# Kernel tuning notes

Measured on AMD Instinct MI355X. Metric: run time of the kernel, lower is better.

## Reference

```python
import jax, jax.numpy as jnp
from jax import lax
import numpy as np

B, N_MEL, T_MEL = 256, 80, 800
R = 16                      # n_frames_per_step
RNN = 1024                  # decoder_rnn_dim
ENC = 256                   # token_embedding_size
MEL_DIM = N_MEL * R         # 1280, == RNN + ENC (LSTMCell input size)
IN_DIM = RNN + ENC          # 1280


def setup_inputs() -> dict:
    key = jax.random.key(0)
    ks = jax.random.split(key, 10)
    s = 0.02
    return {
        "context": jax.random.normal(ks[0], (B, ENC), dtype=jnp.float32),
        "target": jax.random.normal(ks[1], (B, N_MEL, T_MEL), dtype=jnp.float32),
        "W_ih": jax.random.normal(ks[2], (4 * RNN, IN_DIM), dtype=jnp.float32) * s,
        "b_ih": jnp.zeros((4 * RNN,), dtype=jnp.float32),
        "W_hh": jax.random.normal(ks[3], (4 * RNN, RNN), dtype=jnp.float32) * s,
        "b_hh": jnp.zeros((4 * RNN,), dtype=jnp.float32),
        "W_proj": jax.random.normal(ks[4], (MEL_DIM, IN_DIM), dtype=jnp.float32) * s,
        "b_proj": jnp.zeros((MEL_DIM,), dtype=jnp.float32),
        "W_gate": jax.random.normal(ks[5], (1, IN_DIM), dtype=jnp.float32) * s,
        "b_gate": jnp.zeros((1,), dtype=jnp.float32),
    }


def _decoder_forward(context, target, W_ih, b_ih, W_hh, b_hh, W_proj, b_proj, W_gate, b_gate):
    b = context.shape[0]
    n_mel, t_mel = target.shape[1], target.shape[2]
    mel_dim = W_proj.shape[0]
    r = mel_dim // n_mel                      # n_frames_per_step
    T = t_mel // r                            # decoder steps
    rnn = W_hh.shape[1]

    # parse_decoder_inputs: [B, n_mel, T_mel] -> [T, B, mel_dim]
    frames = target.transpose(0, 2, 1).reshape(b, T, mel_dim).transpose(1, 0, 2)
    # step 0 uses the all-zeros go frame; step t>=1 uses target frame t (teacher forcing, p=1)
    inputs = frames.at[0].set(0.0)

    h0 = jnp.zeros((b, rnn), dtype=context.dtype)
    c0 = jnp.zeros((b, rnn), dtype=context.dtype)

    def step(carry, x):
        h, c = carry
        gates = x @ W_ih.T + b_ih + h @ W_hh.T + b_hh   # [B, 4*rnn]
        i, f, g, o = jnp.split(gates, 4, axis=-1)        # torch LSTMCell gate order
        c_new = jax.nn.sigmoid(f) * c + jax.nn.sigmoid(i) * jnp.tanh(g)
        h_new = jax.nn.sigmoid(o) * jnp.tanh(c_new)
        # eval mode: dropout on c is identity
        oc = jnp.concatenate([h_new, context], axis=1)   # [B, rnn+enc]
        mel = oc @ W_proj.T + b_proj                     # [B, mel_dim]
        gate = oc @ W_gate.T + b_gate                    # [B, 1]
        return (h_new, c_new), (mel, gate)

    _, (mels, gates) = lax.scan(step, (h0, c0), inputs)
    # mels: [T, B, mel_dim] -> [B, n_mel, T_mel]
    mel_outputs = mels.transpose(1, 0, 2).reshape(b, T * r, n_mel).transpose(0, 2, 1)
    gate_outputs = gates.transpose(1, 0, 2)              # [B, T, 1]
    return mel_outputs, gate_outputs


def reference(context, target, W_ih, b_ih, W_hh, b_hh, W_proj, b_proj, W_gate, b_gate):
    return _decoder_forward(context, target, W_ih, b_ih, W_hh, b_hh,
                            W_proj, b_proj, W_gate, b_gate)
```

## Files before the change

kernel.cpp:

```cpp
#include <hip/hip_runtime.h>
#include <hip/hip_bf16.h>
#include <math.h>

#define BB     256
#define NMEL   80
#define TMEL   800
#define NFR    16
#define TT     50
#define RNN    1024
#define ENC    256
#define INDIM  1280
#define G4     4096
#define MROWS  (TT*BB)

typedef __attribute__((ext_vector_type(8))) short bf16x8;
typedef __attribute__((ext_vector_type(4))) float f32x4;

#define GAS __attribute__((address_space(1)))
#define LAS __attribute__((address_space(3)))

__device__ __forceinline__ unsigned short f2bf(float f) {
    unsigned int u = __float_as_uint(f);
    u += 0x7FFFu + ((u >> 16) & 1u);
    return (unsigned short)(u >> 16);
}
__device__ __forceinline__ float bf2f(unsigned short s) {
    return __uint_as_float(((unsigned int)s) << 16);
}
__device__ __forceinline__ float fsig(float x) {
    return 1.f / (1.f + __expf(-x));
}
__device__ __forceinline__ float ftanh(float x) {
    return 2.f / (1.f + __expf(-2.f * x)) - 1.f;
}


__global__ void k_f32_to_bf16(const float* __restrict__ src,
                              unsigned short* __restrict__ dst, int n) {
    for (int i = blockIdx.x * blockDim.x + threadIdx.x; i < n;
         i += gridDim.x * blockDim.x)
        dst[i] = f2bf(src[i]);
}

__global__ void k_conv_wph(const float* __restrict__ wproj,
                           unsigned short* __restrict__ dst) {
    const int n = INDIM * RNN;
    for (int i = blockIdx.x * blockDim.x + threadIdx.x; i < n;
         i += gridDim.x * blockDim.x) {
        int mp = i >> 10, k = i & 1023;
        int mel = mp >> 4, fr = mp & 15;
        dst[i] = f2bf(wproj[(fr * NMEL + mel) * INDIM + k]);
    }
}

__global__ void k_frames(const float* __restrict__ target,
                         unsigned short* __restrict__ frames) {
    const int n = TT * BB * INDIM;
    for (int i = blockIdx.x * blockDim.x + threadIdx.x; i < n;
         i += gridDim.x * blockDim.x) {
        int k = i % INDIM;
        int rb = i / INDIM;
        int b = rb & (BB - 1);
        int t = rb >> 8;
        unsigned short v = 0;
        if (t > 0) {
            int mel = k % NMEL, fr = k / NMEL;
            v = f2bf(target[(b * NMEL + mel) * TMEL + t * NFR + fr]);
        }
        frames[i] = v;
    }
}

__global__ void k_ctxproj(const float* __restrict__ context,
                          const float* __restrict__ wproj,
                          const float* __restrict__ bproj,
                          float* __restrict__ ctx) {
    int i = blockIdx.x * blockDim.x + threadIdx.x;
    if (i >= BB * INDIM) return;
    int mp = i % INDIM, b = i / INDIM;
    int mel = mp >> 4, fr = mp & 15;
    int m = fr * NMEL + mel;
    const float* wr = wproj + (size_t)m * INDIM + RNN;
    const float* cb = context + b * ENC;
    float acc = bproj[m];
    for (int e = 0; e < ENC; ++e) acc += cb[e] * wr[e];
    ctx[(size_t)b * INDIM + mp] = acc;
}

__global__ void k_gatectx(const float* __restrict__ context,
                          const float* __restrict__ wgate,
                          const float* __restrict__ bgate,
                          float* __restrict__ gctx) {
    int b = blockIdx.x * blockDim.x + threadIdx.x;
    if (b >= BB) return;
    float acc = bgate[0];
    const float* cb = context + b * ENC;
    for (int e = 0; e < ENC; ++e) acc += cb[e] * wgate[RNN + e];
    gctx[b] = acc;
}

template<int STRIDE, int KDIM>
__device__ __forceinline__ void gemm_core2(const unsigned short* __restrict__ A,
                                           const unsigned short* __restrict__ Bw,
                                           int mblk, int nblk,
                                           unsigned short* As,
                                           unsigned short* Bs,
                                           f32x4 acc[4][2]) {
    const int tid = threadIdx.x, lane = tid & 63, w = tid >> 6;
    const int lr = lane & 15, q = lane >> 4;
    const int wm = (w >> 2) * 64, wn = (w & 3) * 32;
    const int cc1 = tid, cc2 = tid + 512;
    const int r1 = cc1 >> 3, s1 = ((cc1 & 7) ^ (r1 & 7)) * 8;
    const int r2 = cc2 >> 3, s2 = ((cc2 & 7) ^ (r2 & 7)) * 8;
    const unsigned short* a1p = A + (size_t)(mblk + r1) * STRIDE + s1;
    const unsigned short* a2p = A + (size_t)(mblk + r2) * STRIDE + s2;
    const unsigned short* b1p = Bw + (size_t)(nblk + r1) * STRIDE + s1;
    const unsigned short* b2p = Bw + (size_t)(nblk + r2) * STRIDE + s2;

#define GSTAGE(buf, k0) do {                                                   \
    __builtin_amdgcn_global_load_lds((const GAS unsigned int*)(a1p + (k0)),    \
        (LAS unsigned int*)(As + (buf) * 8192 + w * 512), 16, 0, 0);           \
    __builtin_amdgcn_global_load_lds((const GAS unsigned int*)(a2p + (k0)),    \
        (LAS unsigned int*)(As + (buf) * 8192 + 4096 + w * 512), 16, 0, 0);    \
    __builtin_amdgcn_global_load_lds((const GAS unsigned int*)(b1p + (k0)),    \
        (LAS unsigned int*)(Bs + (buf) * 8192 + w * 512), 16, 0, 0);           \
    __builtin_amdgcn_global_load_lds((const GAS unsigned int*)(b2p + (k0)),    \
        (LAS unsigned int*)(Bs + (buf) * 8192 + 4096 + w * 512), 16, 0, 0); } while (0)

    constexpr int NIT = KDIM / 64;
    GSTAGE(0, 0);
    #pragma unroll 4
    for (int it = 0; it < NIT; ++it) {
        if (it < NIT - 1) {
            GSTAGE((it + 1) & 1, (it + 1) * 64);
            asm volatile("s_waitcnt vmcnt(4)" ::: "memory");
        } else {
            asm volatile("s_waitcnt vmcnt(0)" ::: "memory");
        }
        asm volatile("s_barrier" ::: "memory");
        __builtin_amdgcn_sched_barrier(0);
        const unsigned short* Ab = As + (it & 1) * 8192;
        const unsigned short* Bb = Bs + (it & 1) * 8192;
        #pragma unroll
        for (int ks = 0; ks < 2; ++ks) {
            const int j = (((ks * 4 + q) ^ (lr & 7)) * 8);
            bf16x8 af[4], bv[2];
            #pragma unroll
            for (int mi = 0; mi < 4; ++mi)
                af[mi] = *(const bf16x8*)(Ab + (wm + mi * 16 + lr) * 64 + j);
            #pragma unroll
            for (int ni = 0; ni < 2; ++ni)
                bv[ni] = *(const bf16x8*)(Bb + (wn + ni * 16 + lr) * 64 + j);
            #pragma unroll
            for (int mi = 0; mi < 4; ++mi)
                #pragma unroll
                for (int ni = 0; ni < 2; ++ni)
                    acc[mi][ni] = __builtin_amdgcn_mfma_f32_16x16x32_bf16(
                        af[mi], bv[ni], acc[mi][ni], 0, 0, 0);
        }
        asm volatile("s_waitcnt lgkmcnt(0)" ::: "memory");
        __builtin_amdgcn_sched_barrier(0);
        asm volatile("s_barrier" ::: "memory");
    }
#undef GSTAGE
}

__global__ __launch_bounds__(512) void k_gemm_xproj(
    const unsigned short* __restrict__ A,
    const unsigned short* __restrict__ Bw,
    const float* __restrict__ b_ih, const float* __restrict__ b_hh,
    unsigned short* __restrict__ Cout)
{
    __shared__ unsigned short As[2][8192], Bs[2][8192];
    f32x4 acc[4][2] = {};
    const int mblk = blockIdx.y * 128, nblk = blockIdx.x * 128;
    gemm_core2<INDIM, INDIM>(A, Bw, mblk, nblk, &As[0][0], &Bs[0][0], acc);
    const int lane = threadIdx.x & 63, w = threadIdx.x >> 6;
    const int wm = (w >> 2) * 64, wn = (w & 3) * 32;
    const int lr = lane & 15, q = lane >> 4;
    #pragma unroll
    for (int ni = 0; ni < 2; ++ni) {
        const int col = nblk + wn + ni * 16 + lr;
        const float bias = b_ih[col] + b_hh[col];
        #pragma unroll
        for (int mi = 0; mi < 4; ++mi) {
            const int row0 = mblk + wm + mi * 16 + q * 4;
            #pragma unroll
            for (int r = 0; r < 4; ++r)
                Cout[(size_t)(row0 + r) * G4 + col] = f2bf(acc[mi][ni][r] + bias);
        }
    }
}

__global__ __launch_bounds__(512) void k_gemm_mel(
    const unsigned short* __restrict__ A,
    const unsigned short* __restrict__ Bw,
    const float* __restrict__ ctxproj,
    float* __restrict__ out0)
{
    __shared__ unsigned short As[2][8192], Bs[2][8192];
    __shared__ float txp[8][16][20];
    f32x4 acc[4][2] = {};
    const int mblk = blockIdx.y * 128, nblk = blockIdx.x * 128;
    gemm_core2<RNN, RNN>(A, Bw, mblk, nblk, &As[0][0], &Bs[0][0], acc);
    const int lane = threadIdx.x & 63, w = threadIdx.x >> 6;
    const int wm = (w >> 2) * 64, wn = (w & 3) * 32;
    const int lr = lane & 15, q = lane >> 4;
    const int rbase = q * 4;
    const int rowl = lane & 15, fq = lane >> 4;
    #pragma unroll
    for (int mi = 0; mi < 4; ++mi) {
        const int row0 = mblk + wm + mi * 16;
        const int t = row0 >> 8, b0 = row0 & 255;
        #pragma unroll
        for (int ni = 0; ni < 2; ++ni) {
            const int colbase = nblk + wn + ni * 16;
            const int mel = colbase >> 4;
            __syncthreads();
            #pragma unroll
            for (int r = 0; r < 4; ++r)
                txp[w][rbase + r][lr] = acc[mi][ni][r];
            __syncthreads();
            const int bL = b0 + rowl;
            f32x4 v = *(const f32x4*)&txp[w][rowl][fq * 4];
            f32x4 cx = *(const f32x4*)(ctxproj + (size_t)bL * INDIM +
                                       mel * 16 + fq * 4);
            *(f32x4*)(out0 + (size_t)(bL * NMEL + mel) * TMEL +
                      t * NFR + fq * 4) = v + cx;
        }
    }
}

__global__ __launch_bounds__(512) void k_step(
    const unsigned short* __restrict__ Whh,
    const unsigned short* __restrict__ xproj_t,
    const unsigned short* __restrict__ h_prev,
    unsigned short* __restrict__ h_next,
    float* __restrict__ c)
{
    __shared__ unsigned short Abuf[3][8192];
    __shared__ unsigned short Bbuf[3][8192];
    __shared__ unsigned short xg[4096];
    __shared__ float cld[64][16];
    __shared__ float gates[4][64][17];
    const int tid = threadIdx.x, lane = tid & 63, w = tid >> 6;
    const int g = w & 3, mh = w >> 2;
    const int n0 = blockIdx.x * 16, m0 = blockIdx.y * 64;
    const int lr = lane & 15, q = lane >> 4;

    const int cc1 = tid, cc2 = tid + 512;
    const int r1 = cc1 >> 4, s1g = (cc1 & 15) ^ (r1 & 15);
    const int r2 = cc2 >> 4, s2g = (cc2 & 15) ^ (r2 & 15);
    const unsigned short* a1src = h_prev + (size_t)(m0 + r1) * RNN + s1g * 8;
    const unsigned short* a2src = h_prev + (size_t)(m0 + r2) * RNN + s2g * 8;
    const unsigned short* b1src = Whh +
        (size_t)((r1 >> 4) * RNN + n0 + (r1 & 15)) * RNN + s1g * 8;
    const unsigned short* b2src = Whh +
        (size_t)((r2 >> 4) * RNN + n0 + (r2 & 15)) * RNN + s2g * 8;
    const unsigned short* xsrc = xproj_t +
        (size_t)(m0 + ((tid >> 1) & 63)) * G4 + (tid >> 7) * RNN + n0 +
        (tid & 1) * 8;
    const float* csrc = c + (size_t)(m0 + (tid >> 2)) * RNN + n0 + (tid & 3) * 4;

#define STAGE(buf, k0) do {                                                    \
    __builtin_amdgcn_global_load_lds((const GAS unsigned int*)(a1src + (k0)),  \
        (LAS unsigned int*)&Abuf[buf][w * 512], 16, 0, 0);                     \
    __builtin_amdgcn_global_load_lds((const GAS unsigned int*)(a2src + (k0)),  \
        (LAS unsigned int*)&Abuf[buf][4096 + w * 512], 16, 0, 0);              \
    __builtin_amdgcn_global_load_lds((const GAS unsigned int*)(b1src + (k0)),  \
        (LAS unsigned int*)&Bbuf[buf][w * 512], 16, 0, 0);                     \
    __builtin_amdgcn_global_load_lds((const GAS unsigned int*)(b2src + (k0)),  \
        (LAS unsigned int*)&Bbuf[buf][4096 + w * 512], 16, 0, 0); } while (0)

    if (w < 4)
        __builtin_amdgcn_global_load_lds((const GAS unsigned int*)csrc,
            (LAS unsigned int*)&cld[w * 16][0], 16, 0, 0);
    __builtin_amdgcn_global_load_lds((const GAS unsigned int*)xsrc,
        (LAS unsigned int*)&xg[w * 512], 16, 0, 0);
    STAGE(0, 0); STAGE(1, 128);

    f32x4 acc[2] = {};
    #pragma unroll
    for (int it = 0; it < 8; ++it) {
        if (it <= 5) STAGE((it + 2) % 3, (it + 2) * 128);
        if (it <= 5)      asm volatile("s_waitcnt vmcnt(8)" ::: "memory");
        else if (it == 6) asm volatile("s_waitcnt vmcnt(4)" ::: "memory");
        else              asm volatile("s_waitcnt vmcnt(0)" ::: "memory");
        asm volatile("s_barrier" ::: "memory");
        __builtin_amdgcn_sched_barrier(0);
        const unsigned short* Ab = Abuf[it % 3];
        const unsigned short* Bb = Bbuf[it % 3];
        #pragma unroll
        for (int ks = 0; ks < 4; ++ks) {
            const int j = ((ks * 4 + q) ^ lr) * 8;
            bf16x8 a0 = *(const bf16x8*)(Ab + (mh * 32 + lr) * 128 + j);
            bf16x8 a1 = *(const bf16x8*)(Ab + (mh * 32 + 16 + lr) * 128 + j);
            bf16x8 bv = *(const bf16x8*)(Bb + (g * 16 + lr) * 128 + j);
            acc[0] = __builtin_amdgcn_mfma_f32_16x16x32_bf16(a0, bv, acc[0], 0, 0, 0);
            acc[1] = __builtin_amdgcn_mfma_f32_16x16x32_bf16(a1, bv, acc[1], 0, 0, 0);
        }
        asm volatile("s_waitcnt lgkmcnt(0)" ::: "memory");
        __builtin_amdgcn_sched_barrier(0);
        asm volatile("s_barrier" ::: "memory");
    }

    #pragma unroll
    for (int mi = 0; mi < 2; ++mi)
        #pragma unroll
        for (int r = 0; r < 4; ++r) {
            const int row = mh * 32 + mi * 16 + q * 4 + r;
            gates[g][row][lr] = acc[mi][r] +
                bf2f(xg[(g * 64 + row) * 16 + lr]);
        }
    __syncthreads();

    #pragma unroll
    for (int q2 = 0; q2 < 2; ++q2) {
        const int e = tid + q2 * 512;
        const int row = e >> 4, col = e & 15;
        const int b = m0 + row, j = n0 + col;
        const float xi = gates[0][row][col];
        const float xf = gates[1][row][col];
        const float xgt = gates[2][row][col];
        const float xo = gates[3][row][col];
        const float si = fsig(xi);
        const float sf = fsig(xf);
        const float so = fsig(xo);
        const float cp = cld[row][col];
        const float cn = sf * cp + si * ftanh(xgt);
        const float hn = so * ftanh(cn);
        c[(size_t)b * RNN + j] = cn;
        h_next[(size_t)b * RNN + j] = f2bf(hn);
    }
#undef STAGE
}

__global__ void k_gate(const unsigned short* __restrict__ h,
                       const float* __restrict__ wgate,
                       const float* __restrict__ gctx,
                       float* __restrict__ out1) {
    const int gw = (blockIdx.x * blockDim.x + threadIdx.x) >> 6;
    const int lane = threadIdx.x & 63;
    if (gw >= MROWS) return;
    const unsigned short* hr = h + (size_t)gw * RNN + lane * 16;
    const float* wr = wgate + lane * 16;
    float acc = 0.f;
    #pragma unroll
    for (int j = 0; j < 16; ++j) acc += bf2f(hr[j]) * wr[j];
    for (int off = 32; off; off >>= 1) acc += __shfl_down(acc, off);
    if (lane == 0) {
        const int t = gw >> 8, b = gw & 255;
        out1[b * TT + t] = acc + gctx[b];
    }
}

static const size_t OFF_WIH   = 0;
static const size_t OFF_WHH   = OFF_WIH   + (size_t)G4 * INDIM * 2;
static const size_t OFF_WPH   = OFF_WHH   + (size_t)G4 * RNN * 2;
static const size_t OFF_FRM   = OFF_WPH   + (size_t)INDIM * RNN * 2;
static const size_t OFF_XPROJ = OFF_FRM   + (size_t)MROWS * INDIM * 2;
static const size_t OFF_HALL  = OFF_XPROJ + (size_t)MROWS * G4 * 2;
static const size_t OFF_C     = OFF_HALL  + (size_t)(TT + 1) * BB * RNN * 2;
static const size_t OFF_CTX   = OFF_C     + (size_t)BB * RNN * 4;
static const size_t OFF_GCTX  = OFF_CTX   + (size_t)BB * INDIM * 4;

extern "C" void kernel_launch(void* const* d_in, const int* in_sizes, int n_in,
                              void* d_out, int out_size, void* d_ws, size_t ws_size,
                              hipStream_t stream) {
    const float* context = (const float*)d_in[0];
    const float* target  = (const float*)d_in[1];
    const float* W_ih    = (const float*)d_in[2];
    const float* b_ih    = (const float*)d_in[3];
    const float* W_hh    = (const float*)d_in[4];
    const float* b_hh    = (const float*)d_in[5];
    const float* W_proj  = (const float*)d_in[6];
    const float* b_proj  = (const float*)d_in[7];
    const float* W_gate  = (const float*)d_in[8];
    const float* b_gate  = (const float*)d_in[9];
    float* out = (float*)d_out;
    char* ws = (char*)d_ws;

    unsigned short* wih_bf  = (unsigned short*)(ws + OFF_WIH);
    unsigned short* whh_bf  = (unsigned short*)(ws + OFF_WHH);
    unsigned short* wph_bf  = (unsigned short*)(ws + OFF_WPH);
    unsigned short* frames  = (unsigned short*)(ws + OFF_FRM);
    unsigned short* xproj   = (unsigned short*)(ws + OFF_XPROJ);
    unsigned short* h_all   = (unsigned short*)(ws + OFF_HALL);
    float*          c_buf   = (float*)(ws + OFF_C);
    float*          ctxproj = (float*)(ws + OFF_CTX);
    float*          gctx    = (float*)(ws + OFF_GCTX);

    hipMemsetAsync(h_all, 0, (size_t)BB * RNN * 2, stream);
    hipMemsetAsync(c_buf, 0, (size_t)BB * RNN * 4, stream);

    k_f32_to_bf16<<<2048, 256, 0, stream>>>(W_ih, wih_bf, G4 * INDIM);
    k_f32_to_bf16<<<2048, 256, 0, stream>>>(W_hh, whh_bf, G4 * RNN);
    k_conv_wph<<<2048, 256, 0, stream>>>(W_proj, wph_bf);
    k_frames<<<2048, 256, 0, stream>>>(target, frames);
    k_ctxproj<<<(BB * INDIM + 255) / 256, 256, 0, stream>>>(context, W_proj,
                                                            b_proj, ctxproj);
    k_gatectx<<<1, 256, 0, stream>>>(context, W_gate, b_gate, gctx);

    k_gemm_xproj<<<dim3(G4 / 128, MROWS / 128), 512, 0, stream>>>(
        frames, wih_bf, b_ih, b_hh, xproj);

    for (int t = 0; t < TT; ++t) {
        k_step<<<dim3(64, 4), 512, 0, stream>>>(
            whh_bf, xproj + (size_t)t * BB * G4,
            h_all + (size_t)t * BB * RNN,
            h_all + (size_t)(t + 1) * BB * RNN, c_buf);
    }

    k_gemm_mel<<<dim3(INDIM / 128, MROWS / 128), 512, 0, stream>>>(
        h_all + (size_t)BB * RNN, wph_bf, ctxproj, out);
    k_gate<<<MROWS / 4, 256, 0, stream>>>(h_all + (size_t)BB * RNN, W_gate,
                                          gctx, out + (size_t)BB * NMEL * TMEL);
}
```

Measured before the change: 825.1 us.

## Restructure recurrent step kernel and vectorize preprocessing conversion kernels

The per-timestep LSTM kernel drops from 512 to 256 threads. It now uses a 4-deep pipeline with a K-chunk of 64, and each wave computes all four gates for its own 16 rows. This lets the cell update run directly from registers, without the shared-memory gates buffer and its extra barrier. The weight conversion kernels now use vector loads and stores, frames are built through a shared-memory transpose with coalesced reads, and two syncthreads in the mel epilogue are removed, since each wave only touches its own txp slice. The main risk is the reworked waitcnt and barrier ordering around the deeper LDS ring.

```diff
diff --git a/kernel.cpp b/kernel.cpp
--- a/kernel.cpp
+++ b/kernel.cpp
@@ -36,38 +36,67 @@
 
 
 __global__ void k_f32_to_bf16(const float* __restrict__ src,
-                              unsigned short* __restrict__ dst, int n) {
-    for (int i = blockIdx.x * blockDim.x + threadIdx.x; i < n;
-         i += gridDim.x * blockDim.x)
-        dst[i] = f2bf(src[i]);
+                              unsigned short* __restrict__ dst, int n4) {
+    for (int i = blockIdx.x * blockDim.x + threadIdx.x; i < n4;
+         i += gridDim.x * blockDim.x) {
+        f32x4 v = *(const f32x4*)(src + (size_t)i * 4);
+        unsigned long long p = (unsigned long long)f2bf(v[0]) |
+                               ((unsigned long long)f2bf(v[1]) << 16) |
+                               ((unsigned long long)f2bf(v[2]) << 32) |
+                               ((unsigned long long)f2bf(v[3]) << 48);
+        *(unsigned long long*)(dst + (size_t)i * 4) = p;
+    }
 }
 
 __global__ void k_conv_wph(const float* __restrict__ wproj,
                            unsigned short* __restrict__ dst) {
-    const int n = INDIM * RNN;
-    for (int i = blockIdx.x * blockDim.x + threadIdx.x; i < n;
+    const int n4 = INDIM * RNN / 4;
+    for (int i = blockIdx.x * blockDim.x + threadIdx.x; i < n4;
          i += gridDim.x * blockDim.x) {
-        int mp = i >> 10, k = i & 1023;
+        int mp = i >> 8, kc = (i & 255) * 4;
         int mel = mp >> 4, fr = mp & 15;
-        dst[i] = f2bf(wproj[(fr * NMEL + mel) * INDIM + k]);
-    }
-}
-
-__global__ void k_frames(const float* __restrict__ target,
-                         unsigned short* __restrict__ frames) {
-    const int n = TT * BB * INDIM;
-    for (int i = blockIdx.x * blockDim.x + threadIdx.x; i < n;
-         i += gridDim.x * blockDim.x) {
-        int k = i % INDIM;
-        int rb = i / INDIM;
-        int b = rb & (BB - 1);
-        int t = rb >> 8;
-        unsigned short v = 0;
-        if (t > 0) {
-            int mel = k % NMEL, fr = k / NMEL;
-            v = f2bf(target[(b * NMEL + mel) * TMEL + t * NFR + fr]);
-        }
-        frames[i] = v;
+        f32x4 v = *(const f32x4*)(wproj + (size_t)(fr * NMEL + mel) * INDIM + kc);
+        unsigned long long p = (unsigned long long)f2bf(v[0]) |
+                               ((unsigned long long)f2bf(v[1]) << 16) |
+                               ((unsigned long long)f2bf(v[2]) << 32) |
+                               ((unsigned long long)f2bf(v[3]) << 48);
+        *(unsigned long long*)(dst + (size_t)i * 4) = p;
+    }
+}
+
+__global__ __launch_bounds__(128) void k_frames(const float* __restrict__ target,
+                                                unsigned short* __restrict__ frames) {
+    const int wg = blockIdx.x;
+    const int t = wg >> 8, b = wg & 255;
+    unsigned short* dst = frames + ((size_t)t * BB + b) * INDIM;
+    if (t == 0) {
+        for (int i = threadIdx.x; i < INDIM / 8; i += 128)
+            *(f32x4*)(dst + i * 8) = (f32x4){0.f, 0.f, 0.f, 0.f};
+        return;
+    }
+    __shared__ float ld[NMEL][17];
+    for (int i = threadIdx.x; i < 320; i += 128) {
+        const int mel = i >> 2, fq = i & 3;
+        f32x4 v = *(const f32x4*)(target + ((size_t)b * NMEL + mel) * TMEL +
+                                  t * NFR + fq * 4);
+        #pragma unroll
+        for (int j = 0; j < 4; ++j) ld[mel][fq * 4 + j] = v[j];
+    }
+    __syncthreads();
+    for (int i = threadIdx.x; i < 160; i += 128) {
+        unsigned long long p0 = 0, p1 = 0;
+        #pragma unroll
+        for (int j = 0; j < 4; ++j) {
+            const int k = i * 8 + j;
+            p0 |= (unsigned long long)f2bf(ld[k % 80][k / 80]) << (16 * j);
+        }
+        #pragma unroll
+        for (int j = 0; j < 4; ++j) {
+            const int k = i * 8 + 4 + j;
+            p1 |= (unsigned long long)f2bf(ld[k % 80][k / 80]) << (16 * j);
+        }
+        *(unsigned long long*)(dst + i * 8) = p0;
+        *(unsigned long long*)(dst + i * 8 + 4) = p1;
     }
 }
 
@@ -216,11 +245,9 @@
         for (int ni = 0; ni < 2; ++ni) {
             const int colbase = nblk + wn + ni * 16;
             const int mel = colbase >> 4;
-            __syncthreads();
             #pragma unroll
             for (int r = 0; r < 4; ++r)
                 txp[w][rbase + r][lr] = acc[mi][ni][r];
-            __syncthreads();
             const int bL = b0 + rowl;
             f32x4 v = *(const f32x4*)&txp[w][rowl][fq * 4];
             f32x4 cx = *(const f32x4*)(ctxproj + (size_t)bL * INDIM +
@@ -231,106 +258,96 @@
     }
 }
 
-__global__ __launch_bounds__(512) void k_step(
+__global__ __launch_bounds__(256) void k_step(
     const unsigned short* __restrict__ Whh,
     const unsigned short* __restrict__ xproj_t,
     const unsigned short* __restrict__ h_prev,
     unsigned short* __restrict__ h_next,
     float* __restrict__ c)
 {
-    __shared__ unsigned short Abuf[3][8192];
-    __shared__ unsigned short Bbuf[3][8192];
+    __shared__ unsigned short Abuf[4][4096];
+    __shared__ unsigned short Bbuf[4][4096];
     __shared__ unsigned short xg[4096];
     __shared__ float cld[64][16];
-    __shared__ float gates[4][64][17];
     const int tid = threadIdx.x, lane = tid & 63, w = tid >> 6;
-    const int g = w & 3, mh = w >> 2;
     const int n0 = blockIdx.x * 16, m0 = blockIdx.y * 64;
     const int lr = lane & 15, q = lane >> 4;
 
-    const int cc1 = tid, cc2 = tid + 512;
-    const int r1 = cc1 >> 4, s1g = (cc1 & 15) ^ (r1 & 15);
-    const int r2 = cc2 >> 4, s2g = (cc2 & 15) ^ (r2 & 15);
-    const unsigned short* a1src = h_prev + (size_t)(m0 + r1) * RNN + s1g * 8;
-    const unsigned short* a2src = h_prev + (size_t)(m0 + r2) * RNN + s2g * 8;
+    const int cc1 = tid, cc2 = tid + 256;
+    const int r1 = cc1 >> 3, s1 = ((cc1 & 7) ^ (r1 & 7)) * 8;
+    const int r2 = cc2 >> 3, s2 = ((cc2 & 7) ^ (r2 & 7)) * 8;
+    const unsigned short* a1src = h_prev + (size_t)(m0 + r1) * RNN + s1;
+    const unsigned short* a2src = h_prev + (size_t)(m0 + r2) * RNN + s2;
     const unsigned short* b1src = Whh +
-        (size_t)((r1 >> 4) * RNN + n0 + (r1 & 15)) * RNN + s1g * 8;
+        (size_t)((r1 >> 4) * RNN + n0 + (r1 & 15)) * RNN + s1;
     const unsigned short* b2src = Whh +
-        (size_t)((r2 >> 4) * RNN + n0 + (r2 & 15)) * RNN + s2g * 8;
-    const unsigned short* xsrc = xproj_t +
-        (size_t)(m0 + ((tid >> 1) & 63)) * G4 + (tid >> 7) * RNN + n0 +
-        (tid & 1) * 8;
+        (size_t)((r2 >> 4) * RNN + n0 + (r2 & 15)) * RNN + s2;
+    const unsigned short* xs1 = xproj_t +
+        (size_t)(m0 + ((cc1 >> 1) & 63)) * G4 + (cc1 >> 7) * RNN + n0 + (cc1 & 1) * 8;
+    const unsigned short* xs2 = xproj_t +
+        (size_t)(m0 + ((cc2 >> 1) & 63)) * G4 + (cc2 >> 7) * RNN + n0 + (cc2 & 1) * 8;
     const float* csrc = c + (size_t)(m0 + (tid >> 2)) * RNN + n0 + (tid & 3) * 4;
 
 #define STAGE(buf, k0) do {                                                    \
     __builtin_amdgcn_global_load_lds((const GAS unsigned int*)(a1src + (k0)),  \
         (LAS unsigned int*)&Abuf[buf][w * 512], 16, 0, 0);                     \
     __builtin_amdgcn_global_load_lds((const GAS unsigned int*)(a2src + (k0)),  \
-        (LAS unsigned int*)&Abuf[buf][4096 + w * 512], 16, 0, 0);              \
+        (LAS unsigned int*)&Abuf[buf][2048 + w * 512], 16, 0, 0);              \
     __builtin_amdgcn_global_load_lds((const GAS unsigned int*)(b1src + (k0)),  \
         (LAS unsigned int*)&Bbuf[buf][w * 512], 16, 0, 0);                     \
     __builtin_amdgcn_global_load_lds((const GAS unsigned int*)(b2src + (k0)),  \
-        (LAS unsigned int*)&Bbuf[buf][4096 + w * 512], 16, 0, 0); } while (0)
-
-    if (w < 4)
-        __builtin_amdgcn_global_load_lds((const GAS unsigned int*)csrc,
-            (LAS unsigned int*)&cld[w * 16][0], 16, 0, 0);
-    __builtin_amdgcn_global_load_lds((const GAS unsigned int*)xsrc,
+        (LAS unsigned int*)&Bbuf[buf][2048 + w * 512], 16, 0, 0); } while (0)
+
+    __builtin_amdgcn_global_load_lds((const GAS unsigned int*)xs1,
         (LAS unsigned int*)&xg[w * 512], 16, 0, 0);
-    STAGE(0, 0); STAGE(1, 128);
-
-    f32x4 acc[2] = {};
+    __builtin_amdgcn_global_load_lds((const GAS unsigned int*)xs2,
+        (LAS unsigned int*)&xg[2048 + w * 512], 16, 0, 0);
+    __builtin_amdgcn_global_load_lds((const GAS unsigned int*)csrc,
+        (LAS unsigned int*)&cld[w * 16][0], 16, 0, 0);
+    STAGE(0, 0); STAGE(1, 64); STAGE(2, 128);
+
+    f32x4 acc[4] = {};
     #pragma unroll
-    for (int it = 0; it < 8; ++it) {
-        if (it <= 5) STAGE((it + 2) % 3, (it + 2) * 128);
-        if (it <= 5)      asm volatile("s_waitcnt vmcnt(8)" ::: "memory");
-        else if (it == 6) asm volatile("s_waitcnt vmcnt(4)" ::: "memory");
-        else              asm volatile("s_waitcnt vmcnt(0)" ::: "memory");
+    for (int it = 0; it < 16; ++it) {
+        if (it <= 13)      asm volatile("s_waitcnt vmcnt(8)" ::: "memory");
+        else if (it == 14) asm volatile("s_waitcnt vmcnt(4)" ::: "memory");
+        else               asm volatile("s_waitcnt vmcnt(0)" ::: "memory");
+        asm volatile("s_waitcnt lgkmcnt(0)" ::: "memory");
         asm volatile("s_barrier" ::: "memory");
         __builtin_amdgcn_sched_barrier(0);
-        const unsigned short* Ab = Abuf[it % 3];
-        const unsigned short* Bb = Bbuf[it % 3];
-        #pragma unroll
-        for (int ks = 0; ks < 4; ++ks) {
-            const int j = ((ks * 4 + q) ^ lr) * 8;
-            bf16x8 a0 = *(const bf16x8*)(Ab + (mh * 32 + lr) * 128 + j);
-            bf16x8 a1 = *(const bf16x8*)(Ab + (mh * 32 + 16 + lr) * 128 + j);
-            bf16x8 bv = *(const bf16x8*)(Bb + (g * 16 + lr) * 128 + j);
-            acc[0] = __builtin_amdgcn_mfma_f32_16x16x32_bf16(a0, bv, acc[0], 0, 0, 0);
-            acc[1] = __builtin_amdgcn_mfma_f32_16x16x32_bf16(a1, bv, acc[1], 0, 0, 0);
-        }
-        asm volatile("s_waitcnt lgkmcnt(0)" ::: "memory");
-        __builtin_amdgcn_sched_barrier(0);
-        asm volatile("s_barrier" ::: "memory");
+        if (it <= 12) STAGE((it + 3) & 3, (it + 3) * 64);
+        const unsigned short* Ab = Abuf[it & 3];
+        const unsigned short* Bb = Bbuf[it & 3];
+        #pragma unroll
+        for (int ks = 0; ks < 2; ++ks) {
+            const int j = (((ks * 4 + q) ^ (lr & 7)) * 8);
+            bf16x8 av = *(const bf16x8*)(Ab + (w * 16 + lr) * 64 + j);
+            bf16x8 b0 = *(const bf16x8*)(Bb + (lr) * 64 + j);
+            bf16x8 b1 = *(const bf16x8*)(Bb + (16 + lr) * 64 + j);
+            bf16x8 b2 = *(const bf16x8*)(Bb + (32 + lr) * 64 + j);
+            bf16x8 b3 = *(const bf16x8*)(Bb + (48 + lr) * 64 + j);
+            acc[0] = __builtin_amdgcn_mfma_f32_16x16x32_bf16(av, b0, acc[0], 0, 0, 0);
+            acc[1] = __builtin_amdgcn_mfma_f32_16x16x32_bf16(av, b1, acc[1], 0, 0, 0);
+            acc[2] = __builtin_amdgcn_mfma_f32_16x16x32_bf16(av, b2, acc[2], 0, 0, 0);
+            acc[3] = __builtin_amdgcn_mfma_f32_16x16x32_bf16(av, b3, acc[3], 0, 0, 0);
+        }
     }
 
     #pragma unroll
-    for (int mi = 0; mi < 2; ++mi)
-        #pragma unroll
-        for (int r = 0; r < 4; ++r) {
-            const int row = mh * 32 + mi * 16 + q * 4 + r;
-            gates[g][row][lr] = acc[mi][r] +
-                bf2f(xg[(g * 64 + row) * 16 + lr]);
-        }
-    __syncthreads();
-
-    #pragma unroll
-    for (int q2 = 0; q2 < 2; ++q2) {
-        const int e = tid + q2 * 512;
-        const int row = e >> 4, col = e & 15;
-        const int b = m0 + row, j = n0 + col;
-        const float xi = gates[0][row][col];
-        const float xf = gates[1][row][col];
-        const float xgt = gates[2][row][col];
-        const float xo = gates[3][row][col];
+    for (int r = 0; r < 4; ++r) {
+        const int row = w * 16 + q * 4 + r;
+        const float xi = acc[0][r] + bf2f(xg[(0 * 64 + row) * 16 + lr]);
+        const float xf = acc[1][r] + bf2f(xg[(1 * 64 + row) * 16 + lr]);
+        const float xgt = acc[2][r] + bf2f(xg[(2 * 64 + row) * 16 + lr]);
+        const float xo = acc[3][r] + bf2f(xg[(3 * 64 + row) * 16 + lr]);
         const float si = fsig(xi);
         const float sf = fsig(xf);
         const float so = fsig(xo);
-        const float cp = cld[row][col];
+        const float cp = cld[row][lr];
         const float cn = sf * cp + si * ftanh(xgt);
         const float hn = so * ftanh(cn);
-        c[(size_t)b * RNN + j] = cn;
-        h_next[(size_t)b * RNN + j] = f2bf(hn);
+        c[(size_t)(m0 + row) * RNN + n0 + lr] = cn;
+        h_next[(size_t)(m0 + row) * RNN + n0 + lr] = f2bf(hn);
     }
 #undef STAGE
 }
@@ -393,10 +410,10 @@
     hipMemsetAsync(h_all, 0, (size_t)BB * RNN * 2, stream);
     hipMemsetAsync(c_buf, 0, (size_t)BB * RNN * 4, stream);
 
-    k_f32_to_bf16<<<2048, 256, 0, stream>>>(W_ih, wih_bf, G4 * INDIM);
-    k_f32_to_bf16<<<2048, 256, 0, stream>>>(W_hh, whh_bf, G4 * RNN);
+    k_f32_to_bf16<<<2048, 256, 0, stream>>>(W_ih, wih_bf, G4 * INDIM / 4);
+    k_f32_to_bf16<<<2048, 256, 0, stream>>>(W_hh, whh_bf, G4 * RNN / 4);
     k_conv_wph<<<2048, 256, 0, stream>>>(W_proj, wph_bf);
-    k_frames<<<2048, 256, 0, stream>>>(target, frames);
+    k_frames<<<MROWS, 128, 0, stream>>>(target, frames);
     k_ctxproj<<<(BB * INDIM + 255) / 256, 256, 0, stream>>>(context, W_proj,
                                                             b_proj, ctxproj);
     k_gatectx<<<1, 256, 0, stream>>>(context, W_gate, b_gate, gctx);
@@ -405,7 +422,7 @@
         frames, wih_bf, b_ih, b_hh, xproj);
 
     for (int t = 0; t < TT; ++t) {
-        k_step<<<dim3(64, 4), 512, 0, stream>>>(
+        k_step<<<dim3(64, 4), 256, 0, stream>>>(
             whh_bf, xproj + (size_t)t * BB * G4,
             h_all + (size_t)t * BB * RNN,
             h_all + (size_t)(t + 1) * BB * RNN, c_buf);
```

Result: slower. 860.2 us (+4.3%).

## Vectorize conversion kernels, tile frame transpose via LDS, restructure step pipeline barriers

Applied to the files above, without the earlier changes.

The weight conversion kernels now read four floats per thread and write packed 64-bit bf16 stores. The frame-packing kernel gives each (t,b) row its own block, loads coalesced 16-frame chunks into shared memory, and writes packed bf16 output instead of doing strided scalar gathers. The mel GEMM epilogue drops two __syncthreads per tile, which relies on each wave only touching its own txp slot. The step kernel issues its next-stage prefetch after a single barrier per iteration instead of before it, removing the trailing barrier but changing the vmcnt wait counts and prefetch timing.

```diff
diff --git a/kernel.cpp b/kernel.cpp
--- a/kernel.cpp
+++ b/kernel.cpp
@@ -36,38 +36,67 @@
 
 
 __global__ void k_f32_to_bf16(const float* __restrict__ src,
-                              unsigned short* __restrict__ dst, int n) {
-    for (int i = blockIdx.x * blockDim.x + threadIdx.x; i < n;
-         i += gridDim.x * blockDim.x)
-        dst[i] = f2bf(src[i]);
+                              unsigned short* __restrict__ dst, int n4) {
+    for (int i = blockIdx.x * blockDim.x + threadIdx.x; i < n4;
+         i += gridDim.x * blockDim.x) {
+        f32x4 v = *(const f32x4*)(src + (size_t)i * 4);
+        unsigned long long p = (unsigned long long)f2bf(v[0]) |
+                               ((unsigned long long)f2bf(v[1]) << 16) |
+                               ((unsigned long long)f2bf(v[2]) << 32) |
+                               ((unsigned long long)f2bf(v[3]) << 48);
+        *(unsigned long long*)(dst + (size_t)i * 4) = p;
+    }
 }
 
 __global__ void k_conv_wph(const float* __restrict__ wproj,
                            unsigned short* __restrict__ dst) {
-    const int n = INDIM * RNN;
-    for (int i = blockIdx.x * blockDim.x + threadIdx.x; i < n;
+    const int n4 = INDIM * RNN / 4;
+    for (int i = blockIdx.x * blockDim.x + threadIdx.x; i < n4;
          i += gridDim.x * blockDim.x) {
-        int mp = i >> 10, k = i & 1023;
+        int mp = i >> 8, kc = (i & 255) * 4;
         int mel = mp >> 4, fr = mp & 15;
-        dst[i] = f2bf(wproj[(fr * NMEL + mel) * INDIM + k]);
-    }
-}
-
-__global__ void k_frames(const float* __restrict__ target,
-                         unsigned short* __restrict__ frames) {
-    const int n = TT * BB * INDIM;
-    for (int i = blockIdx.x * blockDim.x + threadIdx.x; i < n;
-         i += gridDim.x * blockDim.x) {
-        int k = i % INDIM;
-        int rb = i / INDIM;
-        int b = rb & (BB - 1);
-        int t = rb >> 8;
-        unsigned short v = 0;
-        if (t > 0) {
-            int mel = k % NMEL, fr = k / NMEL;
-            v = f2bf(target[(b * NMEL + mel) * TMEL + t * NFR + fr]);
-        }
-        frames[i] = v;
+        f32x4 v = *(const f32x4*)(wproj + (size_t)(fr * NMEL + mel) * INDIM + kc);
+        unsigned long long p = (unsigned long long)f2bf(v[0]) |
+                               ((unsigned long long)f2bf(v[1]) << 16) |
+                               ((unsigned long long)f2bf(v[2]) << 32) |
+                               ((unsigned long long)f2bf(v[3]) << 48);
+        *(unsigned long long*)(dst + (size_t)i * 4) = p;
+    }
+}
+
+__global__ __launch_bounds__(128) void k_frames(const float* __restrict__ target,
+                                                unsigned short* __restrict__ frames) {
+    const int wg = blockIdx.x;
+    const int t = wg >> 8, b = wg & 255;
+    unsigned short* dst = frames + ((size_t)t * BB + b) * INDIM;
+    if (t == 0) {
+        for (int i = threadIdx.x; i < INDIM / 8; i += 128)
+            *(f32x4*)(dst + i * 8) = (f32x4){0.f, 0.f, 0.f, 0.f};
+        return;
+    }
+    __shared__ float ld[NMEL][17];
+    for (int i = threadIdx.x; i < 320; i += 128) {
+        const int mel = i >> 2, fq = i & 3;
+        f32x4 v = *(const f32x4*)(target + ((size_t)b * NMEL + mel) * TMEL +
+                                  t * NFR + fq * 4);
+        #pragma unroll
+        for (int j = 0; j < 4; ++j) ld[mel][fq * 4 + j] = v[j];
+    }
+    __syncthreads();
+    for (int i = threadIdx.x; i < 160; i += 128) {
+        unsigned long long p0 = 0, p1 = 0;
+        #pragma unroll
+        for (int j = 0; j < 4; ++j) {
+            const int k = i * 8 + j;
+            p0 |= (unsigned long long)f2bf(ld[k % 80][k / 80]) << (16 * j);
+        }
+        #pragma unroll
+        for (int j = 0; j < 4; ++j) {
+            const int k = i * 8 + 4 + j;
+            p1 |= (unsigned long long)f2bf(ld[k % 80][k / 80]) << (16 * j);
+        }
+        *(unsigned long long*)(dst + i * 8) = p0;
+        *(unsigned long long*)(dst + i * 8 + 4) = p1;
     }
 }
 
@@ -216,11 +245,9 @@
         for (int ni = 0; ni < 2; ++ni) {
             const int colbase = nblk + wn + ni * 16;
             const int mel = colbase >> 4;
-            __syncthreads();
             #pragma unroll
             for (int r = 0; r < 4; ++r)
                 txp[w][rbase + r][lr] = acc[mi][ni][r];
-            __syncthreads();
             const int bL = b0 + rowl;
             f32x4 v = *(const f32x4*)&txp[w][rowl][fq * 4];
             f32x4 cx = *(const f32x4*)(ctxproj + (size_t)bL * INDIM +
@@ -282,12 +309,12 @@
     f32x4 acc[2] = {};
     #pragma unroll
     for (int it = 0; it < 8; ++it) {
-        if (it <= 5) STAGE((it + 2) % 3, (it + 2) * 128);
-        if (it <= 5)      asm volatile("s_waitcnt vmcnt(8)" ::: "memory");
-        else if (it == 6) asm volatile("s_waitcnt vmcnt(4)" ::: "memory");
-        else              asm volatile("s_waitcnt vmcnt(0)" ::: "memory");
+        if (it <= 6) asm volatile("s_waitcnt vmcnt(4)" ::: "memory");
+        else         asm volatile("s_waitcnt vmcnt(0)" ::: "memory");
+        asm volatile("s_waitcnt lgkmcnt(0)" ::: "memory");
         asm volatile("s_barrier" ::: "memory");
         __builtin_amdgcn_sched_barrier(0);
+        if (it <= 5) STAGE((it + 2) % 3, (it + 2) * 128);
         const unsigned short* Ab = Abuf[it % 3];
         const unsigned short* Bb = Bbuf[it % 3];
         #pragma unroll
@@ -299,9 +326,6 @@
             acc[0] = __builtin_amdgcn_mfma_f32_16x16x32_bf16(a0, bv, acc[0], 0, 0, 0);
             acc[1] = __builtin_amdgcn_mfma_f32_16x16x32_bf16(a1, bv, acc[1], 0, 0, 0);
         }
-        asm volatile("s_waitcnt lgkmcnt(0)" ::: "memory");
-        __builtin_amdgcn_sched_barrier(0);
-        asm volatile("s_barrier" ::: "memory");
     }
 
     #pragma unroll
@@ -393,10 +417,10 @@
     hipMemsetAsync(h_all, 0, (size_t)BB * RNN * 2, stream);
     hipMemsetAsync(c_buf, 0, (size_t)BB * RNN * 4, stream);
 
-    k_f32_to_bf16<<<2048, 256, 0, stream>>>(W_ih, wih_bf, G4 * INDIM);
-    k_f32_to_bf16<<<2048, 256, 0, stream>>>(W_hh, whh_bf, G4 * RNN);
+    k_f32_to_bf16<<<2048, 256, 0, stream>>>(W_ih, wih_bf, G4 * INDIM / 4);
+    k_f32_to_bf16<<<2048, 256, 0, stream>>>(W_hh, whh_bf, G4 * RNN / 4);
     k_conv_wph<<<2048, 256, 0, stream>>>(W_proj, wph_bf);
-    k_frames<<<2048, 256, 0, stream>>>(target, frames);
+    k_frames<<<MROWS, 128, 0, stream>>>(target, frames);
     k_ctxproj<<<(BB * INDIM + 255) / 256, 256, 0, stream>>>(context, W_proj,
                                                             b_proj, ctxproj);
     k_gatectx<<<1, 256, 0, stream>>>(context, W_gate, b_gate, gctx);
```

New measurement: 753.8 us. 8.6% less time.
